# Performance work log

Hardware: AMD Instinct MI355X
Metric: run time of the kernel (lower is better)

## Reference

```python
import jax, jax.numpy as jnp
import numpy as np

B, S, NC, ND, V = 16, 512, 10000, 10000, 128


def _rn(k, shape, scale=0.05):
    return jax.random.normal(k, shape, dtype=jnp.float32) * scale


def setup_inputs() -> dict:
    key = jax.random.key(0)
    ks = jax.random.split(key, 24)
    inp = {
        'c_seq': jax.random.randint(ks[0], (B, S), 0, NC),
        'd_seq': jax.random.randint(ks[1], (B, S), 0, ND),
        'r_seq': jax.random.uniform(ks[2], (B, S), dtype=jnp.float32),
        # embeddings / vectors
        'D1_w': _rn(ks[3], (ND, 1)),
        'D2_w': _rn(ks[4], (ND, V)),
        'v_r': _rn(ks[5], (V,)),
        'v_beta': _rn(ks[6], (V,)),
        # GRU (torch layout: gates ordered r,z,n; W_ih [3V,2V], W_hh [3V,V])
        'W_ih': _rn(ks[7], (3 * V, 2 * V)),
        'W_hh': _rn(ks[8], (3 * V, V)),
        'b_ih': jnp.zeros((3 * V,), jnp.float32),
        'b_hh': jnp.zeros((3 * V,), jnp.float32),
        # linear_1: V -> V -> V -> 1 (weights stored [in, out])
        'm1_W1': _rn(ks[9], (V, V)), 'm1_b1': jnp.zeros((V,), jnp.float32),
        'm1_W2': _rn(ks[10], (V, V)), 'm1_b2': jnp.zeros((V,), jnp.float32),
        'm1_W3': _rn(ks[11], (V, 1)), 'm1_b3': jnp.zeros((1,), jnp.float32),
        # linear_2: 3V -> V -> V -> 1
        'm2_W1': _rn(ks[12], (3 * V, V)), 'm2_b1': jnp.zeros((V,), jnp.float32),
        'm2_W2': _rn(ks[13], (V, V)), 'm2_b2': jnp.zeros((V,), jnp.float32),
        'm2_W3': _rn(ks[14], (V, 1)), 'm2_b3': jnp.zeros((1,), jnp.float32),
    }
    return inp


def _mlp(x, W1, b1, W2, b2, W3, b3):
    h = jax.nn.relu(x @ W1 + b1)
    h = jax.nn.relu(h @ W2 + b2)
    return h @ W3 + b3


def _gru_seq(x, W_ih, W_hh, b_ih, b_hh):
    # x: [B,S,2V] -> h_seq [B,S,V]; torch GRU gate order r,z,n
    xp = x @ W_ih.T + b_ih  # [B,S,3V]

    def step(h, xt):
        hp = h @ W_hh.T + b_hh
        xr, xz, xn = jnp.split(xt, 3, axis=-1)
        hr, hz, hn = jnp.split(hp, 3, axis=-1)
        r = jax.nn.sigmoid(xr + hr)
        z = jax.nn.sigmoid(xz + hz)
        n = jnp.tanh(xn + r * hn)
        h_new = (1.0 - z) * n + z * h
        return h_new, h_new

    h0 = jnp.zeros((x.shape[0], W_hh.shape[1]), x.dtype)
    _, hs = jax.lax.scan(step, h0, jnp.swapaxes(xp, 0, 1))  # [S,B,V]
    return jnp.swapaxes(hs, 0, 1)


def reference(c_seq, d_seq, r_seq, D1_w, D2_w, v_r, v_beta,
              W_ih, W_hh, b_ih, b_hh,
              m1_W1, m1_b1, m1_W2, m1_b2, m1_W3, m1_b3,
              m2_W1, m2_b1, m2_W2, m2_b2, m2_W3, m2_b3):
    v_d_seq = D2_w[d_seq]                     # [B,S,V]
    v_r_seq = r_seq[..., None] * v_r          # [B,S,V]

    h_seq = _gru_seq(jnp.concatenate([v_d_seq, v_r_seq], axis=-1),
                     W_ih, W_hh, b_ih, b_hh)  # [B,S,V]
    alpha_seq = _mlp(h_seq, m1_W1, m1_b1, m1_W2, m1_b2, m1_W3, m1_b3)[..., 0]  # [B,S]

    bidx = jnp.arange(c_seq.shape[0])

    def step(C, ins):
        c_t, vd_t, vr_t = ins                 # [B], [B,V], [B,V]
        beta_prev = C[bidx, c_t]              # gather: [B]
        v_beta_prev = beta_prev[:, None] * v_beta  # [B,V]
        new_c = _mlp(jnp.concatenate([v_beta_prev, vd_t, vr_t], axis=-1),
                     m2_W1, m2_b1, m2_W2, m2_b2, m2_W3, m2_b3)[:, 0]  # [B]
        C = C.at[bidx, c_t].set(new_c)        # scatter
        return C, (C, new_c)

    C0 = jnp.zeros((c_seq.shape[0], NC), jnp.float32)
    _, (C_seq, beta_seq) = jax.lax.scan(
        step, C0,
        (jnp.swapaxes(c_seq, 0, 1), jnp.swapaxes(v_d_seq, 0, 1), jnp.swapaxes(v_r_seq, 0, 1)))
    C_seq = jnp.swapaxes(C_seq, 0, 1)[..., None]   # [B,S,NC,1]
    beta_seq = jnp.swapaxes(beta_seq, 0, 1)        # [B,S]

    gamma_seq = D1_w[d_seq][..., 0]                # [B,S]
    return (alpha_seq, beta_seq, gamma_seq, h_seq, C_seq)
```

## Files before the change

kernel.cpp:

```cpp
#include <hip/hip_runtime.h>

#define Bq   16
#define Sq   512
#define Vq   128
#define NCq  10000

typedef __attribute__((ext_vector_type(8))) short short8v;
typedef __attribute__((ext_vector_type(4))) float f32x4;

#define OFF_XPF    0u
#define OFF_P1F    3145728u
#define OFF_WTIH   4194304u
#define OFF_WVRIH  4243456u
#define OFF_WVR1   4243840u
#define OFF_WVB    4243968u
#define OFF_PO     4244096u

#define PLN 136
#define PLSZ (16*PLN+8)

__device__ __forceinline__ unsigned cvt_pk_bf16(float a, float b) {
    unsigned r;
    asm("v_cvt_pk_bf16_f32 %0, %1, %2" : "=v"(r) : "v"(a), "v"(b));
    return r;
}
__device__ __forceinline__ void barrier_lgkm() {
    asm volatile("s_waitcnt lgkmcnt(0)" ::: "memory");
    __builtin_amdgcn_sched_barrier(0);
    __builtin_amdgcn_s_barrier();
    __builtin_amdgcn_sched_barrier(0);
}
__device__ __forceinline__ void wait_vm4() {
    asm volatile("s_waitcnt vmcnt(4)" ::: "memory");
    __builtin_amdgcn_sched_barrier(0);
}
__device__ __forceinline__ void wait_vm2() {
    asm volatile("s_waitcnt vmcnt(2)" ::: "memory");
    __builtin_amdgcn_sched_barrier(0);
}
__device__ __forceinline__ void gload_lds16(const void* g, void* l) {
    __builtin_amdgcn_global_load_lds(
        (const __attribute__((address_space(1))) unsigned int*)g,
        (__attribute__((address_space(3))) unsigned int*)l, 16, 0, 0);
}

__global__ __launch_bounds__(256) void k0_prep(
    const int* __restrict__ c_seq, const int* __restrict__ d_seq,
    const float* __restrict__ D1_w,
    const float* __restrict__ W_ih,
    const float* __restrict__ v_r, const float* __restrict__ v_beta,
    const float* __restrict__ m2W1,
    float* __restrict__ ws, float* __restrict__ gamma_out)
{
    const int blk = blockIdx.x, tid = threadIdx.x;

    if (blk < 128) {
        float* WTIH = ws + OFF_WTIH;
        int base = blk * 384;
        for (int i = tid; i < 384; i += 256) {
            int e = base + i;
            int k = e / 384, g = e % 384;
            WTIH[e] = W_ih[g * 256 + k];
        }
    } else if (blk == 128) {
        float* WVRIH = ws + OFF_WVRIH;
        float* WVR1  = ws + OFF_WVR1;
        float* WVB   = ws + OFF_WVB;
        for (int g = tid; g < 384; g += 256) {
            float a = 0.f;
            for (int k = 0; k < 128; ++k) a = fmaf(v_r[k], W_ih[g * 256 + 128 + k], a);
            WVRIH[g] = a;
        }
        if (tid < 128) {
            float a = 0.f, b = 0.f;
            for (int k = 0; k < 128; ++k) {
                a = fmaf(v_r[k],    m2W1[(256 + k) * 128 + tid], a);
                b = fmaf(v_beta[k], m2W1[k * 128 + tid],         b);
            }
            WVR1[tid] = a; WVB[tid] = b;
        }
    } else if (blk < 145) {
        const int b = blk - 129;
        __shared__ int cs[Sq];
        for (int i = tid; i < Sq; i += 256) cs[i] = c_seq[b * Sq + i];
        __syncthreads();
        int* PO = (int*)(ws + OFF_PO);
        for (int t = tid; t < Sq; t += 256) {
            int c = cs[t];
            int po = -1;
            for (int u = t - 1; u >= 0; --u) if (cs[u] == c) { po = u; break; }
            PO[t * 16 + b] = po;
        }
    } else {
        const int b = blk - 145;
        for (int s = tid; s < Sq; s += 256)
            gamma_out[b * Sq + s] = D1_w[d_seq[b * Sq + s]];
    }
}

__global__ __launch_bounds__(256) void k1_gemm(
    const int* __restrict__ d_seq, const float* __restrict__ D2_w,
    const float* __restrict__ m2W1,
    const float* __restrict__ b_ih, const float* __restrict__ b_hh,
    const float* __restrict__ r_seq, const float* __restrict__ m2b1,
    float* __restrict__ ws)
{
    __shared__ float As[64 * 128];
    __shared__ float Bs[128 * 64];
    const int blk = blockIdx.x, tid = threadIdx.x;
    const int nc = blk & 7;
    const int m0 = (blk >> 3) * 64;
    const float* WTIH = ws + OFF_WTIH;

    const float4* D2v = (const float4*)D2_w;
    for (int e = tid; e < 2048; e += 256) {
        int r = e >> 5, q = e & 31;
        int d = d_seq[m0 + r];
        *(float4*)&As[r * 128 + 4 * q] = D2v[d * 32 + q];
    }
    for (int e = tid; e < 2048; e += 256) {
        int k = e >> 4, q = e & 15;
        float4 v;
        if (nc < 6) v = *(const float4*)&WTIH[k * 384 + nc * 64 + 4 * q];
        else        v = *(const float4*)&m2W1[(128 + k) * 128 + (nc - 6) * 64 + 4 * q];
        *(float4*)&Bs[k * 64 + 4 * q] = v;
    }
    __syncthreads();

    const int tx = tid & 15, ty = tid >> 4;
    const int c0 = 4 * tx, r0 = 4 * ty;
    float acc[4][4];
#pragma unroll
    for (int i = 0; i < 4; ++i)
#pragma unroll
        for (int j = 0; j < 4; ++j) acc[i][j] = 0.f;

    for (int k = 0; k < 128; ++k) {
        float4 bv = *(const float4*)&Bs[k * 64 + c0];
#pragma unroll
        for (int i = 0; i < 4; ++i) {
            float a = As[(r0 + i) * 128 + k];
            acc[i][0] = fmaf(a, bv.x, acc[i][0]);
            acc[i][1] = fmaf(a, bv.y, acc[i][1]);
            acc[i][2] = fmaf(a, bv.z, acc[i][2]);
            acc[i][3] = fmaf(a, bv.w, acc[i][3]);
        }
    }

    float rsv[4];
#pragma unroll
    for (int i = 0; i < 4; ++i) rsv[i] = r_seq[m0 + r0 + i];

    if (nc < 6) {
        const int grow0 = nc * 64 + c0;
        float4 bi  = *(const float4*)&b_ih[grow0];
        float4 wv4 = *(const float4*)&(ws + OFF_WVRIH)[grow0];
        float4 bh4 = make_float4(0.f, 0.f, 0.f, 0.f);
        if (nc < 4) bh4 = *(const float4*)&b_hh[grow0];
        float* XPF = ws + OFF_XPF;
        const int r4 = grow0 >> 2;
#pragma unroll
        for (int i = 0; i < 4; ++i) {
            int row = m0 + r0 + i;
            int t = row & 511, bb = row >> 9;
            float4 v;
            v.x = acc[i][0] + bi.x + bh4.x + rsv[i] * wv4.x;
            v.y = acc[i][1] + bi.y + bh4.y + rsv[i] * wv4.y;
            v.z = acc[i][2] + bi.z + bh4.z + rsv[i] * wv4.z;
            v.w = acc[i][3] + bi.w + bh4.w + rsv[i] * wv4.w;
            *(float4*)&XPF[((size_t)((bb >> 2) * 512 + t)) * 1536 + r4 * 16 + (bb & 3) * 4] = v;
        }
    } else {
        const int j0 = (nc - 6) * 64 + c0;
        float4 b1v = *(const float4*)&m2b1[j0];
        float4 wr1 = *(const float4*)&(ws + OFF_WVR1)[j0];
        float* P1F = ws + OFF_P1F;
#pragma unroll
        for (int i = 0; i < 4; ++i) {
            int row = m0 + r0 + i;
            int t = row & 511, bb = row >> 9;
            float4 v;
            v.x = acc[i][0] + b1v.x + rsv[i] * wr1.x;
            v.y = acc[i][1] + b1v.y + rsv[i] * wr1.y;
            v.z = acc[i][2] + b1v.z + rsv[i] * wr1.z;
            v.w = acc[i][3] + b1v.w + rsv[i] * wr1.w;
            *(float4*)&P1F[((size_t)(t * 16 + bb)) * 128 + j0] = v;
        }
    }
}

__global__ __launch_bounds__(512, 1) void k2_scan(
    const float* __restrict__ W_hh, const float* __restrict__ b_hh,
    const float* __restrict__ m2W2, const float* __restrict__ m2b2,
    const float* __restrict__ m2W3, const float* __restrict__ m2b3,
    float* __restrict__ ws,
    float* __restrict__ hseq_out, float* __restrict__ beta_out)
{
    __shared__ __align__(16) unsigned char smem[41504];
    const int tid = threadIdx.x;
    const int l = tid & 63, wv = tid >> 6;
    const int qq = l >> 4, cb = l & 15;
    const int bgid = blockIdx.x;

    if (bgid < 4) {
        unsigned short* hP  = (unsigned short*)smem;
        unsigned char*  xsl = smem + 8736;
        const float* XPF = ws + OFF_XPF;

        short8v aH0[4], aH1[4], aH2[4];
#pragma unroll
        for (int kf = 0; kf < 4; ++kf) {
            const int kb = kf * 32 + qq * 8;
            const float* w0 = W_hh + (0 * 128 + 16 * wv + cb) * 128 + kb;
            const float* w1 = W_hh + (1 * 128 + 16 * wv + cb) * 128 + kb;
            const float* w2 = W_hh + (2 * 128 + 16 * wv + cb) * 128 + kb;
            short8v h0, h1, h2;
#pragma unroll
            for (int e = 0; e < 8; ++e) {
                unsigned u0 = __builtin_bit_cast(unsigned, w0[e]);
                unsigned u1 = __builtin_bit_cast(unsigned, w1[e]);
                unsigned u2 = __builtin_bit_cast(unsigned, w2[e]);
                h0[e] = (short)((u0 + 0x7fffu + ((u0 >> 16) & 1u)) >> 16);
                h1[e] = (short)((u1 + 0x7fffu + ((u1 >> 16) & 1u)) >> 16);
                h2[e] = (short)((u2 + 0x7fffu + ((u2 >> 16) & 1u)) >> 16);
            }
            aH0[kf] = h0; aH1[kf] = h1; aH2[kf] = h2;
        }
        f32x4 bhn4;
        {
            float4 t4 = *(const float4*)&b_hh[256 + 16 * wv + 4 * qq];
            bhn4[0] = t4.x; bhn4[1] = t4.y; bhn4[2] = t4.z; bhn4[3] = t4.w;
        }

        float* hp = hseq_out + ((size_t)((bgid * 4 + (cb & 3)) * 512)) * 128 + 16 * wv + 4 * qq;
        float hold[4] = {0.f, 0.f, 0.f, 0.f};
        for (int i = tid; i < 2 * PLSZ; i += 512) hP[i] = 0;
#pragma unroll
        for (int s = 0; s < 3; ++s)
            gload_lds16(XPF + ((size_t)(bgid * 512 + s)) * 1536 + tid * 4,
                        xsl + s * 8192 + tid * 16);
        __syncthreads();

        const float NL2E = -1.44269504f, L2E2 = 2.88539008f;
        for (int t = 0; t < 512; ++t) {
            if (t < 509)
                gload_lds16(XPF + ((size_t)(bgid * 512 + t + 3)) * 1536 + tid * 4,
                            xsl + ((t + 3) & 3) * 8192 + tid * 16);

            const float* xc = (const float*)(xsl + (t & 3) * 8192) +
                              (4 * wv + qq) * 16 + (cb & 3) * 4;
            f32x4 px0 = *(const f32x4*)(xc);
            f32x4 px1 = *(const f32x4*)(xc + 512);
            f32x4 px2 = *(const f32x4*)(xc + 1024);

            const unsigned short* HI = hP + (t & 1) * PLSZ;
            unsigned short* HIn = hP + ((t + 1) & 1) * PLSZ;

            f32x4 C0a = px0, C1a = px1, C2a = bhn4;
            f32x4 C0b = {0.f,0.f,0.f,0.f}, C1b = {0.f,0.f,0.f,0.f}, C2b = {0.f,0.f,0.f,0.f};
            {
                short8v B0 = *(const short8v*)(HI + cb * PLN + 0 * 32 + qq * 8);
                short8v B1 = *(const short8v*)(HI + cb * PLN + 1 * 32 + qq * 8);
                short8v B2 = *(const short8v*)(HI + cb * PLN + 2 * 32 + qq * 8);
                short8v B3 = *(const short8v*)(HI + cb * PLN + 3 * 32 + qq * 8);
                C0a = __builtin_amdgcn_mfma_f32_16x16x32_bf16(aH0[0], B0, C0a, 0, 0, 0);
                C1a = __builtin_amdgcn_mfma_f32_16x16x32_bf16(aH1[0], B0, C1a, 0, 0, 0);
                C2a = __builtin_amdgcn_mfma_f32_16x16x32_bf16(aH2[0], B0, C2a, 0, 0, 0);
                C0b = __builtin_amdgcn_mfma_f32_16x16x32_bf16(aH0[1], B1, C0b, 0, 0, 0);
                C1b = __builtin_amdgcn_mfma_f32_16x16x32_bf16(aH1[1], B1, C1b, 0, 0, 0);
                C2b = __builtin_amdgcn_mfma_f32_16x16x32_bf16(aH2[1], B1, C2b, 0, 0, 0);
                C0a = __builtin_amdgcn_mfma_f32_16x16x32_bf16(aH0[2], B2, C0a, 0, 0, 0);
                C1a = __builtin_amdgcn_mfma_f32_16x16x32_bf16(aH1[2], B2, C1a, 0, 0, 0);
                C2a = __builtin_amdgcn_mfma_f32_16x16x32_bf16(aH2[2], B2, C2a, 0, 0, 0);
                C0b = __builtin_amdgcn_mfma_f32_16x16x32_bf16(aH0[3], B3, C0b, 0, 0, 0);
                C1b = __builtin_amdgcn_mfma_f32_16x16x32_bf16(aH1[3], B3, C1b, 0, 0, 0);
                C2b = __builtin_amdgcn_mfma_f32_16x16x32_bf16(aH2[3], B3, C2b, 0, 0, 0);
            }
            float hnew[4];
#pragma unroll
            for (int i = 0; i < 4; ++i) {
                float pr = C0a[i] + C0b[i];
                float pz = C1a[i] + C1b[i];
                float hn = C2a[i] + C2b[i];
                float r = __builtin_amdgcn_rcpf(1.f + __builtin_amdgcn_exp2f(pr * NL2E));
                float z = __builtin_amdgcn_rcpf(1.f + __builtin_amdgcn_exp2f(pz * NL2E));
                float npre = fmaf(r, hn, px2[i]);
                float n = fmaf(-2.f, __builtin_amdgcn_rcpf(1.f + __builtin_amdgcn_exp2f(npre * L2E2)), 1.f);
                float hv = fmaf(z, hold[i] - n, n);
                hold[i] = hv;
                hnew[i] = hv;
            }
            if (cb < 4) {
                *(float4*)hp = make_float4(hnew[0], hnew[1], hnew[2], hnew[3]);
                uint2 hw;
                hw.x = cvt_pk_bf16(hnew[0], hnew[1]);
                hw.y = cvt_pk_bf16(hnew[2], hnew[3]);
                *(uint2*)(HIn + cb * PLN + 16 * wv + 4 * qq) = hw;
            }
            hp += 128;
            wait_vm4();
            barrier_lgkm();
        }
    } else {
        const int bq = bgid - 4;
        float* bhL = (float*)smem;
        unsigned short* h1P = (unsigned short*)(smem + 8192);
        float* redT = (float*)(smem + 12560);
        unsigned char* psl = smem + 12688;
        const float* P1F = ws + OFF_P1F;
        const int* POg = (const int*)(ws + OFF_PO);

        short8v aH[4];
#pragma unroll
        for (int kf = 0; kf < 4; ++kf) {
            short8v hi;
#pragma unroll
            for (int e = 0; e < 8; ++e) {
                unsigned u = __builtin_bit_cast(unsigned,
                    m2W2[(kf * 32 + qq * 8 + e) * 128 + 16 * wv + cb]);
                hi[e] = (short)((u + 0x7fffu + ((u >> 16) & 1u)) >> 16);
            }
            aH[kf] = hi;
        }
        float w3C[4];
        f32x4 b2C4;
        *(float4*)w3C = *(const float4*)&m2W3[16 * wv + 4 * qq];
        {
            float4 t4 = *(const float4*)&m2b2[16 * wv + 4 * qq];
            b2C4[0] = t4.x; b2C4[1] = t4.y; b2C4[2] = t4.z; b2C4[3] = t4.w;
        }
        const float b3v = m2b3[0];

        const bool pa = (tid < 128);
        const int bb2 = tid & 3, j4 = (tid >> 2) & 31;
        float wvb[4] = {0.f, 0.f, 0.f, 0.f};
        int poCur = -1, poNxt = -1;
        float bpPre = 0.f, btap = 0.f;
        if (pa) {
            *(float4*)wvb = *(const float4*)&(ws + OFF_WVB)[j4 * 4];
            poCur = POg[0 * 16 + 4 * bq + bb2];
            poNxt = POg[1 * 16 + 4 * bq + bb2];
#pragma unroll
            for (int s = 0; s < 3; ++s)
                gload_lds16(P1F + ((size_t)(s * 16 + 4 * bq)) * 128 + tid * 4,
                            psl + s * 2048 + tid * 16);
        }
        for (int i = tid; i < PLSZ; i += 512) h1P[i] = 0;
        __syncthreads();

        for (int t = 0; t < 512; ++t) {
            if (pa) {
                if (t > 0) {
                    float4 ra = *(const float4*)&redT[bb2 * 8];
                    float4 rb = *(const float4*)&redT[bb2 * 8 + 4];
                    btap = ((ra.x + ra.y) + (ra.z + ra.w)) +
                           ((rb.x + rb.y) + (rb.z + rb.w)) + b3v;
                    if (j4 == 0) bhL[bb2 * 512 + (t - 1)] = btap;
                }
                int po = poCur;
                float bp = (po == t - 1) ? btap : bpPre;
                const float* pc = (const float*)(psl + (t & 3) * 2048) + bb2 * 128 + j4 * 4;
                f32x4 p1 = *(const f32x4*)pc;
                float h0 = fmaxf(0.f, fmaf(bp, wvb[0], p1[0]));
                float h1 = fmaxf(0.f, fmaf(bp, wvb[1], p1[1]));
                float h2 = fmaxf(0.f, fmaf(bp, wvb[2], p1[2]));
                float h3 = fmaxf(0.f, fmaf(bp, wvb[3], p1[3]));
                uint2 hw;
                hw.x = cvt_pk_bf16(h0, h1);
                hw.y = cvt_pk_bf16(h2, h3);
                *(uint2*)(h1P + bb2 * PLN + j4 * 4) = hw;
                if (t < 509)
                    gload_lds16(P1F + ((size_t)((t + 3) * 16 + 4 * bq)) * 128 + tid * 4,
                                psl + ((t + 3) & 3) * 2048 + tid * 16);
            }
            barrier_lgkm();

            if (pa) {
                bpPre = 0.f;
                if (poNxt >= 0 && poNxt < t) bpPre = bhL[bb2 * 512 + poNxt];
                poCur = poNxt;
                if (t < 510) poNxt = POg[(t + 2) * 16 + 4 * bq + bb2];
            }
            f32x4 Ca = b2C4, Cb = {0.f, 0.f, 0.f, 0.f};
            {
                short8v B0 = *(const short8v*)(h1P + cb * PLN + 0 * 32 + qq * 8);
                short8v B1 = *(const short8v*)(h1P + cb * PLN + 1 * 32 + qq * 8);
                short8v B2 = *(const short8v*)(h1P + cb * PLN + 2 * 32 + qq * 8);
                short8v B3 = *(const short8v*)(h1P + cb * PLN + 3 * 32 + qq * 8);
                Ca = __builtin_amdgcn_mfma_f32_16x16x32_bf16(aH[0], B0, Ca, 0, 0, 0);
                Cb = __builtin_amdgcn_mfma_f32_16x16x32_bf16(aH[1], B1, Cb, 0, 0, 0);
                Ca = __builtin_amdgcn_mfma_f32_16x16x32_bf16(aH[2], B2, Ca, 0, 0, 0);
                Cb = __builtin_amdgcn_mfma_f32_16x16x32_bf16(aH[3], B3, Cb, 0, 0, 0);
            }
            float part = 0.f;
#pragma unroll
            for (int i = 0; i < 4; ++i)
                part = fmaf(fmaxf(0.f, Ca[i] + Cb[i]), w3C[i], part);
            part += __shfl_xor(part, 16);
            part += __shfl_xor(part, 32);
            if (qq == 0 && cb < 4) redT[cb * 8 + wv] = part;
            wait_vm2();
            barrier_lgkm();
        }
        if (pa) {
            float4 ra = *(const float4*)&redT[bb2 * 8];
            float4 rb = *(const float4*)&redT[bb2 * 8 + 4];
            float bta = ((ra.x + ra.y) + (ra.z + ra.w)) +
                        ((rb.x + rb.y) + (rb.z + rb.w)) + b3v;
            if (j4 == 0) bhL[bb2 * 512 + 511] = bta;
        }
        __syncthreads();
        for (int i = tid; i < 2048; i += 512)
            beta_out[(4 * bq + (i >> 9)) * 512 + (i & 511)] = bhL[i];
    }
}

__global__ __launch_bounds__(256) void k2b_fill(
    const int* __restrict__ c_seq, const float* __restrict__ beta_in,
    float* __restrict__ C_out)
{
    __shared__ int   scs[Sq];
    __shared__ float sbt[Sq];
    const int bid = blockIdx.x, tid = threadIdx.x;
    const int b = bid / 40, rem = bid % 40;
    const int chunk = rem >> 2, q = rem & 3;

    for (int i = tid; i < Sq; i += 256) {
        scs[i] = c_seq[b * Sq + i];
        sbt[i] = beta_in[b * Sq + i];
    }
    __syncthreads();

    const int c0 = chunk * 1024 + tid * 4;
    if (c0 >= NCq) return;

    float cur0 = 0.f, cur1 = 0.f, cur2 = 0.f, cur3 = 0.f;
    const int tlo = q * 128, thi = tlo + 128;
    float* base = C_out + (size_t)b * Sq * NCq + c0;

    for (int t = 0; t < tlo; ++t) {
        int ct = scs[t] - c0; float bv = sbt[t];
        cur0 = (ct == 0) ? bv : cur0;
        cur1 = (ct == 1) ? bv : cur1;
        cur2 = (ct == 2) ? bv : cur2;
        cur3 = (ct == 3) ? bv : cur3;
    }
    for (int t = tlo; t < thi; ++t) {
        int ct = scs[t] - c0; float bv = sbt[t];
        cur0 = (ct == 0) ? bv : cur0;
        cur1 = (ct == 1) ? bv : cur1;
        cur2 = (ct == 2) ? bv : cur2;
        cur3 = (ct == 3) ? bv : cur3;
        *(float4*)(base + (size_t)t * NCq) = make_float4(cur0, cur1, cur2, cur3);
    }
}

__global__ __launch_bounds__(256) void k3_alpha(
    const float* __restrict__ hseq,
    const float* __restrict__ W1, const float* __restrict__ b1,
    const float* __restrict__ W2, const float* __restrict__ b2,
    const float* __restrict__ W3, const float* __restrict__ b3,
    float* __restrict__ alpha_out)
{
    __shared__ float Hs[32 * 128];
    __shared__ float T1[32 * 128];
    __shared__ float red[4][16];
    const int blk = blockIdx.x, tid = threadIdx.x;
    const int row0 = blk * 32;

    for (int e = tid; e < 1024; e += 256) {
        int r = e >> 5, q = e & 31;
        *(float4*)&Hs[r * 128 + 4 * q] =
            *(const float4*)&hseq[(size_t)(row0 + r) * 128 + 4 * q];
    }
    __syncthreads();

    const int j = tid & 127, rh = tid >> 7;
    const float b1j = b1[j], b2j = b2[j], w3j = W3[j];
    float acc[16];
#pragma unroll
    for (int r = 0; r < 16; ++r) acc[r] = b1j;
    for (int k = 0; k < 128; ++k) {
        float w = W1[k * 128 + j];
#pragma unroll
        for (int r = 0; r < 16; ++r)
            acc[r] = fmaf(Hs[(rh * 16 + r) * 128 + k], w, acc[r]);
    }
#pragma unroll
    for (int r = 0; r < 16; ++r) {
        acc[r] = fmaxf(acc[r], 0.f);
        T1[(rh * 16 + r) * 128 + j] = acc[r];
    }
    __syncthreads();
    float acc2[16];
#pragma unroll
    for (int r = 0; r < 16; ++r) acc2[r] = b2j;
    for (int k = 0; k < 128; ++k) {
        float w = W2[k * 128 + j];
#pragma unroll
        for (int r = 0; r < 16; ++r)
            acc2[r] = fmaf(T1[(rh * 16 + r) * 128 + k], w, acc2[r]);
    }
#pragma unroll
    for (int r = 0; r < 16; ++r) {
        float p = fmaxf(acc2[r], 0.f) * w3j;
#pragma unroll
        for (int off = 1; off < 64; off <<= 1) p += __shfl_xor(p, off);
        if ((tid & 63) == 0) red[tid >> 6][r] = p;
    }
    __syncthreads();
    if (tid < 32) {
        int rr = tid & 15, g = tid >> 4;
        alpha_out[row0 + g * 16 + rr] = red[2 * g][rr] + red[2 * g + 1][rr] + b3[0];
    }
}

extern "C" void kernel_launch(void* const* d_in, const int* in_sizes, int n_in,
                              void* d_out, int out_size, void* d_ws, size_t ws_size,
                              hipStream_t stream) {
    const int*   c_seq = (const int*)d_in[0];
    const int*   d_seq = (const int*)d_in[1];
    const float* r_seq = (const float*)d_in[2];
    const float* D1_w  = (const float*)d_in[3];
    const float* D2_w  = (const float*)d_in[4];
    const float* v_r   = (const float*)d_in[5];
    const float* v_b   = (const float*)d_in[6];
    const float* W_ih  = (const float*)d_in[7];
    const float* W_hh  = (const float*)d_in[8];
    const float* b_ih  = (const float*)d_in[9];
    const float* b_hh  = (const float*)d_in[10];
    const float* m1W1  = (const float*)d_in[11];
    const float* m1b1  = (const float*)d_in[12];
    const float* m1W2  = (const float*)d_in[13];
    const float* m1b2  = (const float*)d_in[14];
    const float* m1W3  = (const float*)d_in[15];
    const float* m1b3  = (const float*)d_in[16];
    const float* m2W1  = (const float*)d_in[17];
    const float* m2b1  = (const float*)d_in[18];
    const float* m2W2  = (const float*)d_in[19];
    const float* m2b2  = (const float*)d_in[20];
    const float* m2W3  = (const float*)d_in[21];
    const float* m2b3  = (const float*)d_in[22];

    float* out   = (float*)d_out;
    float* alpha = out;
    float* beta  = out + 8192;
    float* gamma = out + 16384;
    float* hseq  = out + 24576;
    float* Cseq  = out + 1073152;
    float* ws    = (float*)d_ws;

    hipLaunchKernelGGL(k0_prep, dim3(161), dim3(256), 0, stream,
                       c_seq, d_seq, D1_w, W_ih, v_r, v_b, m2W1, ws, gamma);
    hipLaunchKernelGGL(k1_gemm, dim3(1024), dim3(256), 0, stream,
                       d_seq, D2_w, m2W1, b_ih, b_hh, r_seq, m2b1, ws);
    hipLaunchKernelGGL(k2_scan, dim3(8), dim3(512), 0, stream,
                       W_hh, b_hh, m2W2, m2b2, m2W3, m2b3, ws, hseq, beta);
    hipLaunchKernelGGL(k2b_fill, dim3(640), dim3(256), 0, stream,
                       c_seq, beta, Cseq);
    hipLaunchKernelGGL(k3_alpha, dim3(256), dim3(256), 0, stream,
                       hseq, m1W1, m1b1, m1W2, m1b2, m1W3, m1b3, alpha);
}
```

Baseline: 618.8 us.

## Run beta recurrence in a single wavefront covering all batches, removing block barriers

The beta scan moves from four 512-thread blocks, each with two workgroup barriers per timestep and LDS staging, to one 64-lane wavefront that handles all 16 batch rows. The full W2 weight is held in registers as 32 MFMA fragments. P1 is prefetched two steps ahead straight into registers, and the reduction uses shuffles only, so there is no LDS round trip or barrier per step. The grid shrinks from 8 to 5 blocks. The cost is heavy register pressure and a serial chain of 32 MFMAs per step on one wave, where the old version spread that work across waves.

```diff
diff --git a/kernel.cpp b/kernel.cpp
--- a/kernel.cpp
+++ b/kernel.cpp
@@ -32,10 +32,6 @@
 }
 __device__ __forceinline__ void wait_vm4() {
     asm volatile("s_waitcnt vmcnt(4)" ::: "memory");
-    __builtin_amdgcn_sched_barrier(0);
-}
-__device__ __forceinline__ void wait_vm2() {
-    asm volatile("s_waitcnt vmcnt(2)" ::: "memory");
     __builtin_amdgcn_sched_barrier(0);
 }
 __device__ __forceinline__ void gload_lds16(const void* g, void* l) {
@@ -302,116 +298,109 @@
             barrier_lgkm();
         }
     } else {
-        const int bq = bgid - 4;
+        if (tid >= 64) return;
         float* bhL = (float*)smem;
-        unsigned short* h1P = (unsigned short*)(smem + 8192);
-        float* redT = (float*)(smem + 12560);
-        unsigned char* psl = smem + 12688;
         const float* P1F = ws + OFF_P1F;
         const int* POg = (const int*)(ws + OFF_PO);
 
-        short8v aH[4];
-#pragma unroll
-        for (int kf = 0; kf < 4; ++kf) {
-            short8v hi;
-#pragma unroll
-            for (int e = 0; e < 8; ++e) {
-                unsigned u = __builtin_bit_cast(unsigned,
-                    m2W2[(kf * 32 + qq * 8 + e) * 128 + 16 * wv + cb]);
-                hi[e] = (short)((u + 0x7fffu + ((u >> 16) & 1u)) >> 16);
-            }
-            aH[kf] = hi;
-        }
-        float w3C[4];
-        f32x4 b2C4;
-        *(float4*)w3C = *(const float4*)&m2W3[16 * wv + 4 * qq];
-        {
-            float4 t4 = *(const float4*)&m2b2[16 * wv + 4 * qq];
-            b2C4[0] = t4.x; b2C4[1] = t4.y; b2C4[2] = t4.z; b2C4[3] = t4.w;
-        }
+        short8v aH[8][4];
+#pragma unroll
+        for (int m = 0; m < 8; ++m)
+#pragma unroll
+            for (int kf = 0; kf < 4; ++kf) {
+                short8v hi;
+#pragma unroll
+                for (int e = 0; e < 8; ++e) {
+                    unsigned u = __builtin_bit_cast(unsigned,
+                        m2W2[(kf * 32 + qq * 8 + e) * 128 + 16 * m + cb]);
+                    hi[e] = (short)((u + 0x7fffu + ((u >> 16) & 1u)) >> 16);
+                }
+                aH[m][kf] = hi;
+            }
+        f32x4 w3C[8], b2C[8];
+#pragma unroll
+        for (int m = 0; m < 8; ++m) {
+            w3C[m] = __builtin_bit_cast(f32x4, *(const float4*)&m2W3[16 * m + 4 * qq]);
+            b2C[m] = __builtin_bit_cast(f32x4, *(const float4*)&m2b2[16 * m + 4 * qq]);
+        }
+        f32x4 wvb4[8];
+#pragma unroll
+        for (int k2i = 0; k2i < 8; ++k2i)
+            wvb4[k2i] = __builtin_bit_cast(f32x4,
+                *(const float4*)&(ws + OFF_WVB)[(k2i >> 1) * 32 + qq * 8 + (k2i & 1) * 4]);
         const float b3v = m2b3[0];
-
-        const bool pa = (tid < 128);
-        const int bb2 = tid & 3, j4 = (tid >> 2) & 31;
-        float wvb[4] = {0.f, 0.f, 0.f, 0.f};
-        int poCur = -1, poNxt = -1;
-        float bpPre = 0.f, btap = 0.f;
-        if (pa) {
-            *(float4*)wvb = *(const float4*)&(ws + OFF_WVB)[j4 * 4];
-            poCur = POg[0 * 16 + 4 * bq + bb2];
-            poNxt = POg[1 * 16 + 4 * bq + bb2];
-#pragma unroll
-            for (int s = 0; s < 3; ++s)
-                gload_lds16(P1F + ((size_t)(s * 16 + 4 * bq)) * 128 + tid * 4,
-                            psl + s * 2048 + tid * 16);
-        }
-        for (int i = tid; i < PLSZ; i += 512) h1P[i] = 0;
-        __syncthreads();
+        const float* p1base = P1F + cb * 128 + qq * 8;
+
+        f32x4 pA[8], pB[8];
+#pragma unroll
+        for (int k2i = 0; k2i < 8; ++k2i) {
+            pA[k2i] = __builtin_bit_cast(f32x4,
+                *(const float4*)&p1base[(k2i >> 1) * 32 + (k2i & 1) * 4]);
+            pB[k2i] = __builtin_bit_cast(f32x4,
+                *(const float4*)&p1base[2048 + (k2i >> 1) * 32 + (k2i & 1) * 4]);
+        }
+        int poCur = POg[cb];
+        int poNxt = POg[16 + cb];
+        float btap = 0.f, bpPre = 0.f;
 
         for (int t = 0; t < 512; ++t) {
-            if (pa) {
-                if (t > 0) {
-                    float4 ra = *(const float4*)&redT[bb2 * 8];
-                    float4 rb = *(const float4*)&redT[bb2 * 8 + 4];
-                    btap = ((ra.x + ra.y) + (ra.z + ra.w)) +
-                           ((rb.x + rb.y) + (rb.z + rb.w)) + b3v;
-                    if (j4 == 0) bhL[bb2 * 512 + (t - 1)] = btap;
-                }
-                int po = poCur;
-                float bp = (po == t - 1) ? btap : bpPre;
-                const float* pc = (const float*)(psl + (t & 3) * 2048) + bb2 * 128 + j4 * 4;
-                f32x4 p1 = *(const f32x4*)pc;
-                float h0 = fmaxf(0.f, fmaf(bp, wvb[0], p1[0]));
-                float h1 = fmaxf(0.f, fmaf(bp, wvb[1], p1[1]));
-                float h2 = fmaxf(0.f, fmaf(bp, wvb[2], p1[2]));
-                float h3 = fmaxf(0.f, fmaf(bp, wvb[3], p1[3]));
-                uint2 hw;
-                hw.x = cvt_pk_bf16(h0, h1);
-                hw.y = cvt_pk_bf16(h2, h3);
-                *(uint2*)(h1P + bb2 * PLN + j4 * 4) = hw;
-                if (t < 509)
-                    gload_lds16(P1F + ((size_t)((t + 3) * 16 + 4 * bq)) * 128 + tid * 4,
-                                psl + ((t + 3) & 3) * 2048 + tid * 16);
-            }
-            barrier_lgkm();
-
-            if (pa) {
-                bpPre = 0.f;
-                if (poNxt >= 0 && poNxt < t) bpPre = bhL[bb2 * 512 + poNxt];
-                poCur = poNxt;
-                if (t < 510) poNxt = POg[(t + 2) * 16 + 4 * bq + bb2];
-            }
-            f32x4 Ca = b2C4, Cb = {0.f, 0.f, 0.f, 0.f};
-            {
-                short8v B0 = *(const short8v*)(h1P + cb * PLN + 0 * 32 + qq * 8);
-                short8v B1 = *(const short8v*)(h1P + cb * PLN + 1 * 32 + qq * 8);
-                short8v B2 = *(const short8v*)(h1P + cb * PLN + 2 * 32 + qq * 8);
-                short8v B3 = *(const short8v*)(h1P + cb * PLN + 3 * 32 + qq * 8);
-                Ca = __builtin_amdgcn_mfma_f32_16x16x32_bf16(aH[0], B0, Ca, 0, 0, 0);
-                Cb = __builtin_amdgcn_mfma_f32_16x16x32_bf16(aH[1], B1, Cb, 0, 0, 0);
-                Ca = __builtin_amdgcn_mfma_f32_16x16x32_bf16(aH[2], B2, Ca, 0, 0, 0);
-                Cb = __builtin_amdgcn_mfma_f32_16x16x32_bf16(aH[3], B3, Cb, 0, 0, 0);
-            }
+            float bp = (poCur == t - 1) ? btap : bpPre;
+            short8v Bf[4];
+#pragma unroll
+            for (int kf = 0; kf < 4; ++kf) {
+                f32x4 pl = pA[kf * 2], ph = pA[kf * 2 + 1];
+                f32x4 wl = wvb4[kf * 2], wh = wvb4[kf * 2 + 1];
+                float h0 = fmaxf(0.f, fmaf(bp, wl[0], pl[0]));
+                float h1 = fmaxf(0.f, fmaf(bp, wl[1], pl[1]));
+                float h2 = fmaxf(0.f, fmaf(bp, wl[2], pl[2]));
+                float h3 = fmaxf(0.f, fmaf(bp, wl[3], pl[3]));
+                float h4 = fmaxf(0.f, fmaf(bp, wh[0], ph[0]));
+                float h5 = fmaxf(0.f, fmaf(bp, wh[1], ph[1]));
+                float h6 = fmaxf(0.f, fmaf(bp, wh[2], ph[2]));
+                float h7 = fmaxf(0.f, fmaf(bp, wh[3], ph[3]));
+                union { uint4 u; short8v s; } cv;
+                cv.u = make_uint4(cvt_pk_bf16(h0, h1), cvt_pk_bf16(h2, h3),
+                                  cvt_pk_bf16(h4, h5), cvt_pk_bf16(h6, h7));
+                Bf[kf] = cv.s;
+            }
+#pragma unroll
+            for (int k2i = 0; k2i < 8; ++k2i) pA[k2i] = pB[k2i];
+            if (t < 510) {
+#pragma unroll
+                for (int k2i = 0; k2i < 8; ++k2i)
+                    pB[k2i] = __builtin_bit_cast(f32x4,
+                        *(const float4*)&p1base[(size_t)(t + 2) * 2048 +
+                                                (k2i >> 1) * 32 + (k2i & 1) * 4]);
+            }
+            float bpN = 0.f;
+            if (poNxt >= 0 && poNxt < t) bpN = bhL[cb * 512 + poNxt];
+
+            f32x4 C[8];
+#pragma unroll
+            for (int m = 0; m < 8; ++m) C[m] = b2C[m];
+#pragma unroll
+            for (int kf = 0; kf < 4; ++kf)
+#pragma unroll
+                for (int m = 0; m < 8; ++m)
+                    C[m] = __builtin_amdgcn_mfma_f32_16x16x32_bf16(aH[m][kf], Bf[kf], C[m], 0, 0, 0);
+
             float part = 0.f;
 #pragma unroll
-            for (int i = 0; i < 4; ++i)
-                part = fmaf(fmaxf(0.f, Ca[i] + Cb[i]), w3C[i], part);
+            for (int m = 0; m < 8; ++m)
+#pragma unroll
+                for (int i = 0; i < 4; ++i)
+                    part = fmaf(fmaxf(C[m][i], 0.f), w3C[m][i], part);
             part += __shfl_xor(part, 16);
             part += __shfl_xor(part, 32);
-            if (qq == 0 && cb < 4) redT[cb * 8 + wv] = part;
-            wait_vm2();
-            barrier_lgkm();
-        }
-        if (pa) {
-            float4 ra = *(const float4*)&redT[bb2 * 8];
-            float4 rb = *(const float4*)&redT[bb2 * 8 + 4];
-            float bta = ((ra.x + ra.y) + (ra.z + ra.w)) +
-                        ((rb.x + rb.y) + (rb.z + rb.w)) + b3v;
-            if (j4 == 0) bhL[bb2 * 512 + 511] = bta;
-        }
-        __syncthreads();
-        for (int i = tid; i < 2048; i += 512)
-            beta_out[(4 * bq + (i >> 9)) * 512 + (i & 511)] = bhL[i];
+            float bta = part + b3v;
+            if (qq == 0) bhL[cb * 512 + t] = bta;
+            btap = bta;
+            bpPre = bpN;
+            poCur = poNxt;
+            if (t < 510) poNxt = POg[(t + 2) * 16 + cb];
+        }
+        for (int i = tid * 4; i < 8192; i += 256)
+            *(float4*)&beta_out[i] = *(const float4*)&bhL[i];
     }
 }
 
@@ -554,7 +543,7 @@
                        c_seq, d_seq, D1_w, W_ih, v_r, v_b, m2W1, ws, gamma);
     hipLaunchKernelGGL(k1_gemm, dim3(1024), dim3(256), 0, stream,
                        d_seq, D2_w, m2W1, b_ih, b_hh, r_seq, m2b1, ws);
-    hipLaunchKernelGGL(k2_scan, dim3(8), dim3(512), 0, stream,
+    hipLaunchKernelGGL(k2_scan, dim3(5), dim3(512), 0, stream,
                        W_hh, b_hh, m2W2, m2b2, m2W3, m2b3, ws, hseq, beta);
     hipLaunchKernelGGL(k2b_fill, dim3(640), dim3(256), 0, stream,
                        c_seq, beta, Cseq);
```

After: 1.257 ms. 103% more time.

## Split beta recurrence into parallel bulk MLP pass plus sparse repeat-fix pass

Applied to the files above, without the earlier changes.

Before, four blocks in the scan kernel stepped through all 512 beta timesteps in sequence next to the GRU scan. Now 256 extra blocks compute beta for every (b,t) in parallel, assuming the previous beta is zero. That holds whenever the concept c_t has no earlier occurrence. A small follow-up kernel then walks a precomputed list of timesteps whose concept repeats and recomputes only those, in order, using the updated betas. This takes the serial dependency off most steps, at the cost of an extra launch and a serial fp32 fix loop whose length depends on how often concepts repeat.

```diff
diff --git a/kernel.cpp b/kernel.cpp
--- a/kernel.cpp
+++ b/kernel.cpp
@@ -14,7 +14,9 @@
 #define OFF_WVRIH  4243456u
 #define OFF_WVR1   4243840u
 #define OFF_WVB    4243968u
-#define OFF_PO     4244096u
+#define OFF_W2T    4244096u
+#define OFF_LIST   4260480u
+#define OFF_CNT    4276864u
 
 #define PLN 136
 #define PLSZ (16*PLN+8)
@@ -34,10 +36,6 @@
     asm volatile("s_waitcnt vmcnt(4)" ::: "memory");
     __builtin_amdgcn_sched_barrier(0);
 }
-__device__ __forceinline__ void wait_vm2() {
-    asm volatile("s_waitcnt vmcnt(2)" ::: "memory");
-    __builtin_amdgcn_sched_barrier(0);
-}
 __device__ __forceinline__ void gload_lds16(const void* g, void* l) {
     __builtin_amdgcn_global_load_lds(
         (const __attribute__((address_space(1))) unsigned int*)g,
@@ -49,7 +47,7 @@
     const float* __restrict__ D1_w,
     const float* __restrict__ W_ih,
     const float* __restrict__ v_r, const float* __restrict__ v_beta,
-    const float* __restrict__ m2W1,
+    const float* __restrict__ m2W1, const float* __restrict__ m2W2,
     float* __restrict__ ws, float* __restrict__ gamma_out)
 {
     const int blk = blockIdx.x, tid = threadIdx.x;
@@ -82,19 +80,33 @@
     } else if (blk < 145) {
         const int b = blk - 129;
         __shared__ int cs[Sq];
+        __shared__ int po[Sq];
         for (int i = tid; i < Sq; i += 256) cs[i] = c_seq[b * Sq + i];
         __syncthreads();
-        int* PO = (int*)(ws + OFF_PO);
         for (int t = tid; t < Sq; t += 256) {
             int c = cs[t];
-            int po = -1;
-            for (int u = t - 1; u >= 0; --u) if (cs[u] == c) { po = u; break; }
-            PO[t * 16 + b] = po;
-        }
-    } else {
+            int p = -1;
+            for (int u = t - 1; u >= 0; --u) if (cs[u] == c) { p = u; break; }
+            po[t] = p;
+        }
+        __syncthreads();
+        if (tid == 0) {
+            int2* L = (int2*)(ws + OFF_LIST) + b * 512;
+            int n = 0;
+            for (int t = 0; t < Sq; ++t)
+                if (po[t] >= 0) { L[n] = make_int2(t, po[t]); ++n; }
+            ((int*)(ws + OFF_CNT))[b] = n;
+        }
+    } else if (blk < 161) {
         const int b = blk - 145;
         for (int s = tid; s < Sq; s += 256)
             gamma_out[b * Sq + s] = D1_w[d_seq[b * Sq + s]];
+    } else {
+        float* W2T = ws + OFF_W2T;
+        for (int i = tid; i < 16384; i += 256) {
+            int j = i >> 7, k = i & 127;
+            W2T[i] = m2W2[k * 128 + j];
+        }
     }
 }
 
@@ -191,8 +203,8 @@
 
 __global__ __launch_bounds__(512, 1) void k2_scan(
     const float* __restrict__ W_hh, const float* __restrict__ b_hh,
-    const float* __restrict__ m2W2, const float* __restrict__ m2b2,
-    const float* __restrict__ m2W3, const float* __restrict__ m2b3,
+    const float* __restrict__ m2b2, const float* __restrict__ m2W3,
+    const float* __restrict__ m2b3,
     float* __restrict__ ws,
     float* __restrict__ hseq_out, float* __restrict__ beta_out)
 {
@@ -302,116 +314,105 @@
             barrier_lgkm();
         }
     } else {
-        const int bq = bgid - 4;
-        float* bhL = (float*)smem;
-        unsigned short* h1P = (unsigned short*)(smem + 8192);
-        float* redT = (float*)(smem + 12560);
-        unsigned char* psl = smem + 12688;
+        const int d = bgid - 4;
+        float* h1L = (float*)smem;
         const float* P1F = ws + OFF_P1F;
-        const int* POg = (const int*)(ws + OFF_PO);
-
-        short8v aH[4];
-#pragma unroll
-        for (int kf = 0; kf < 4; ++kf) {
-            short8v hi;
-#pragma unroll
-            for (int e = 0; e < 8; ++e) {
-                unsigned u = __builtin_bit_cast(unsigned,
-                    m2W2[(kf * 32 + qq * 8 + e) * 128 + 16 * wv + cb]);
-                hi[e] = (short)((u + 0x7fffu + ((u >> 16) & 1u)) >> 16);
+        const float* W2T = ws + OFF_W2T;
+
+        const float* src = P1F + (size_t)d * 4096;
+        for (int i = tid; i < 1024; i += 512) {
+            float4 v = *(const float4*)&src[i * 4];
+            v.x = fmaxf(v.x, 0.f); v.y = fmaxf(v.y, 0.f);
+            v.z = fmaxf(v.z, 0.f); v.w = fmaxf(v.w, 0.f);
+            *(float4*)&h1L[i * 4] = v;
+        }
+        __syncthreads();
+
+        const int r = tid >> 4, jg = tid & 15;
+        float acc[8];
+#pragma unroll
+        for (int jj = 0; jj < 8; ++jj) acc[jj] = m2b2[jg * 8 + jj];
+        for (int k4 = 0; k4 < 32; ++k4) {
+            float4 h4 = *(const float4*)&h1L[r * 128 + k4 * 4];
+#pragma unroll
+            for (int jj = 0; jj < 8; ++jj) {
+                float4 w4 = *(const float4*)&W2T[(jg * 8 + jj) * 128 + k4 * 4];
+                acc[jj] = fmaf(h4.x, w4.x, acc[jj]);
+                acc[jj] = fmaf(h4.y, w4.y, acc[jj]);
+                acc[jj] = fmaf(h4.z, w4.z, acc[jj]);
+                acc[jj] = fmaf(h4.w, w4.w, acc[jj]);
             }
-            aH[kf] = hi;
-        }
-        float w3C[4];
-        f32x4 b2C4;
-        *(float4*)w3C = *(const float4*)&m2W3[16 * wv + 4 * qq];
-        {
-            float4 t4 = *(const float4*)&m2b2[16 * wv + 4 * qq];
-            b2C4[0] = t4.x; b2C4[1] = t4.y; b2C4[2] = t4.z; b2C4[3] = t4.w;
-        }
-        const float b3v = m2b3[0];
-
-        const bool pa = (tid < 128);
-        const int bb2 = tid & 3, j4 = (tid >> 2) & 31;
-        float wvb[4] = {0.f, 0.f, 0.f, 0.f};
-        int poCur = -1, poNxt = -1;
-        float bpPre = 0.f, btap = 0.f;
-        if (pa) {
-            *(float4*)wvb = *(const float4*)&(ws + OFF_WVB)[j4 * 4];
-            poCur = POg[0 * 16 + 4 * bq + bb2];
-            poNxt = POg[1 * 16 + 4 * bq + bb2];
-#pragma unroll
-            for (int s = 0; s < 3; ++s)
-                gload_lds16(P1F + ((size_t)(s * 16 + 4 * bq)) * 128 + tid * 4,
-                            psl + s * 2048 + tid * 16);
-        }
-        for (int i = tid; i < PLSZ; i += 512) h1P[i] = 0;
-        __syncthreads();
-
-        for (int t = 0; t < 512; ++t) {
-            if (pa) {
-                if (t > 0) {
-                    float4 ra = *(const float4*)&redT[bb2 * 8];
-                    float4 rb = *(const float4*)&redT[bb2 * 8 + 4];
-                    btap = ((ra.x + ra.y) + (ra.z + ra.w)) +
-                           ((rb.x + rb.y) + (rb.z + rb.w)) + b3v;
-                    if (j4 == 0) bhL[bb2 * 512 + (t - 1)] = btap;
-                }
-                int po = poCur;
-                float bp = (po == t - 1) ? btap : bpPre;
-                const float* pc = (const float*)(psl + (t & 3) * 2048) + bb2 * 128 + j4 * 4;
-                f32x4 p1 = *(const f32x4*)pc;
-                float h0 = fmaxf(0.f, fmaf(bp, wvb[0], p1[0]));
-                float h1 = fmaxf(0.f, fmaf(bp, wvb[1], p1[1]));
-                float h2 = fmaxf(0.f, fmaf(bp, wvb[2], p1[2]));
-                float h3 = fmaxf(0.f, fmaf(bp, wvb[3], p1[3]));
-                uint2 hw;
-                hw.x = cvt_pk_bf16(h0, h1);
-                hw.y = cvt_pk_bf16(h2, h3);
-                *(uint2*)(h1P + bb2 * PLN + j4 * 4) = hw;
-                if (t < 509)
-                    gload_lds16(P1F + ((size_t)((t + 3) * 16 + 4 * bq)) * 128 + tid * 4,
-                                psl + ((t + 3) & 3) * 2048 + tid * 16);
-            }
-            barrier_lgkm();
-
-            if (pa) {
-                bpPre = 0.f;
-                if (poNxt >= 0 && poNxt < t) bpPre = bhL[bb2 * 512 + poNxt];
-                poCur = poNxt;
-                if (t < 510) poNxt = POg[(t + 2) * 16 + 4 * bq + bb2];
-            }
-            f32x4 Ca = b2C4, Cb = {0.f, 0.f, 0.f, 0.f};
-            {
-                short8v B0 = *(const short8v*)(h1P + cb * PLN + 0 * 32 + qq * 8);
-                short8v B1 = *(const short8v*)(h1P + cb * PLN + 1 * 32 + qq * 8);
-                short8v B2 = *(const short8v*)(h1P + cb * PLN + 2 * 32 + qq * 8);
-                short8v B3 = *(const short8v*)(h1P + cb * PLN + 3 * 32 + qq * 8);
-                Ca = __builtin_amdgcn_mfma_f32_16x16x32_bf16(aH[0], B0, Ca, 0, 0, 0);
-                Cb = __builtin_amdgcn_mfma_f32_16x16x32_bf16(aH[1], B1, Cb, 0, 0, 0);
-                Ca = __builtin_amdgcn_mfma_f32_16x16x32_bf16(aH[2], B2, Ca, 0, 0, 0);
-                Cb = __builtin_amdgcn_mfma_f32_16x16x32_bf16(aH[3], B3, Cb, 0, 0, 0);
-            }
-            float part = 0.f;
-#pragma unroll
-            for (int i = 0; i < 4; ++i)
-                part = fmaf(fmaxf(0.f, Ca[i] + Cb[i]), w3C[i], part);
-            part += __shfl_xor(part, 16);
-            part += __shfl_xor(part, 32);
-            if (qq == 0 && cb < 4) redT[cb * 8 + wv] = part;
-            wait_vm2();
-            barrier_lgkm();
-        }
-        if (pa) {
-            float4 ra = *(const float4*)&redT[bb2 * 8];
-            float4 rb = *(const float4*)&redT[bb2 * 8 + 4];
-            float bta = ((ra.x + ra.y) + (ra.z + ra.w)) +
-                        ((rb.x + rb.y) + (rb.z + rb.w)) + b3v;
-            if (j4 == 0) bhL[bb2 * 512 + 511] = bta;
-        }
-        __syncthreads();
-        for (int i = tid; i < 2048; i += 512)
-            beta_out[(4 * bq + (i >> 9)) * 512 + (i & 511)] = bhL[i];
+        }
+        float part = 0.f;
+#pragma unroll
+        for (int jj = 0; jj < 8; ++jj)
+            part = fmaf(fmaxf(acc[jj], 0.f), m2W3[jg * 8 + jj], part);
+        part += __shfl_xor(part, 1);
+        part += __shfl_xor(part, 2);
+        part += __shfl_xor(part, 4);
+        part += __shfl_xor(part, 8);
+        if (jg == 0) {
+            int R = d * 32 + r;
+            beta_out[(R & 15) * 512 + (R >> 4)] = part + m2b3[0];
+        }
+    }
+}
+
+__global__ __launch_bounds__(64, 1) void k2c_fix(
+    const float* __restrict__ m2b2, const float* __restrict__ m2W3,
+    const float* __restrict__ m2b3,
+    float* __restrict__ ws, float* __restrict__ beta_out)
+{
+    __shared__ __align__(16) float W2L[128 * 129];
+    __shared__ float betaF[512];
+    __shared__ __align__(16) float h1L[128];
+    const int b = blockIdx.x, l = threadIdx.x;
+    const float* W2T = ws + OFF_W2T;
+    const float* P1F = ws + OFF_P1F;
+
+    for (int i = l; i < 16384; i += 64) {
+        int j = i >> 7, k = i & 127;
+        W2L[j * 129 + k] = W2T[i];
+    }
+    for (int i = l; i < 512; i += 64) betaF[i] = beta_out[b * 512 + i];
+
+    const float2 wvb2 = *(const float2*)&(ws + OFF_WVB)[2 * l];
+    const float2 b22  = *(const float2*)&m2b2[2 * l];
+    const float2 w32  = *(const float2*)&m2W3[2 * l];
+    const float b3v = m2b3[0];
+    const int n = ((const int*)(ws + OFF_CNT))[b];
+    const int2* L = (const int2*)(ws + OFF_LIST) + b * 512;
+    barrier_lgkm();
+
+    for (int i = 0; i < n; ++i) {
+        int2 tp = L[i];
+        float bp = betaF[tp.y];
+        float2 p1 = *(const float2*)&P1F[((size_t)(tp.x * 16 + b)) * 128 + 2 * l];
+        float h0 = fmaxf(0.f, fmaf(bp, wvb2.x, p1.x));
+        float h1 = fmaxf(0.f, fmaf(bp, wvb2.y, p1.y));
+        *(float2*)&h1L[2 * l] = make_float2(h0, h1);
+        barrier_lgkm();
+        float a0 = b22.x, a1 = b22.y;
+        const float* w0 = &W2L[(2 * l) * 129];
+        const float* w1 = &W2L[(2 * l + 1) * 129];
+        for (int k4 = 0; k4 < 32; ++k4) {
+            float4 h4 = *(const float4*)&h1L[k4 * 4];
+            float4 u0 = *(const float4*)&w0[k4 * 4];
+            float4 u1 = *(const float4*)&w1[k4 * 4];
+            a0 = fmaf(h4.x, u0.x, a0); a0 = fmaf(h4.y, u0.y, a0);
+            a0 = fmaf(h4.z, u0.z, a0); a0 = fmaf(h4.w, u0.w, a0);
+            a1 = fmaf(h4.x, u1.x, a1); a1 = fmaf(h4.y, u1.y, a1);
+            a1 = fmaf(h4.z, u1.z, a1); a1 = fmaf(h4.w, u1.w, a1);
+        }
+        float part = fmaf(fmaxf(a0, 0.f), w32.x, fmaxf(a1, 0.f) * w32.y);
+#pragma unroll
+        for (int off = 1; off < 64; off <<= 1) part += __shfl_xor(part, off);
+        float bta = part + b3v;
+        if (l == 0) {
+            betaF[tp.x] = bta;
+            beta_out[b * 512 + tp.x] = bta;
+        }
+        barrier_lgkm();
     }
 }
 
@@ -550,12 +551,14 @@
     float* Cseq  = out + 1073152;
     float* ws    = (float*)d_ws;
 
-    hipLaunchKernelGGL(k0_prep, dim3(161), dim3(256), 0, stream,
-                       c_seq, d_seq, D1_w, W_ih, v_r, v_b, m2W1, ws, gamma);
+    hipLaunchKernelGGL(k0_prep, dim3(162), dim3(256), 0, stream,
+                       c_seq, d_seq, D1_w, W_ih, v_r, v_b, m2W1, m2W2, ws, gamma);
     hipLaunchKernelGGL(k1_gemm, dim3(1024), dim3(256), 0, stream,
                        d_seq, D2_w, m2W1, b_ih, b_hh, r_seq, m2b1, ws);
-    hipLaunchKernelGGL(k2_scan, dim3(8), dim3(512), 0, stream,
-                       W_hh, b_hh, m2W2, m2b2, m2W3, m2b3, ws, hseq, beta);
+    hipLaunchKernelGGL(k2_scan, dim3(260), dim3(512), 0, stream,
+                       W_hh, b_hh, m2b2, m2W3, m2b3, ws, hseq, beta);
+    hipLaunchKernelGGL(k2c_fix, dim3(16), dim3(64), 0, stream,
+                       m2b2, m2W3, m2b3, ws, beta);
     hipLaunchKernelGGL(k2b_fill, dim3(640), dim3(256), 0, stream,
                        c_seq, beta, Cseq);
     hipLaunchKernelGGL(k3_alpha, dim3(256), dim3(256), 0, stream,
```

New measurement: 734.4 us. 1.19x slower.
